# Optimization experiments

Hardware: AMD Instinct MI355X
Metric: run time of the kernel (lower is better)

Reference implementation:

```python
import jax, jax.numpy as jnp
import numpy as np

B, S, E, H = 2, 2048, 1024, 16
HD = E // H
DFF = 4 * E
LN_EPS = 1e-5


def _layernorm(x, g, b):
    mu = jnp.mean(x, axis=-1, keepdims=True)
    var = jnp.mean(jnp.square(x - mu), axis=-1, keepdims=True)
    return (x - mu) * jax.lax.rsqrt(var + LN_EPS) * g + b


def setup_inputs() -> dict:
    key = jax.random.key(0)
    ks = jax.random.split(key, 6)
    inp = {
        "x": jax.random.normal(ks[0], (B, S, E), jnp.float32),
        "ln1_g": jnp.ones((E,), jnp.float32),
        "ln1_b": jnp.zeros((E,), jnp.float32),
        "ln2_g": jnp.ones((E,), jnp.float32),
        "ln2_b": jnp.zeros((E,), jnp.float32),
        # OptimizedPoincareBallLinear init: randn * 0.1, zero bias
        "w_qkv": jax.random.normal(ks[1], (3 * E, E), jnp.float32) * 0.1,
        "b_qkv": jnp.zeros((3 * E,), jnp.float32),
        "w_ao": jax.random.normal(ks[2], (E, E), jnp.float32) * 0.1,
        "b_ao": jnp.zeros((E,), jnp.float32),
        "w_fc": jax.random.normal(ks[3], (DFF, E), jnp.float32) * 0.1,
        "b_fc": jnp.zeros((DFF,), jnp.float32),
        "w_po": jax.random.normal(ks[4], (E, DFF), jnp.float32) * 0.1,
        "b_po": jnp.zeros((E,), jnp.float32),
    }
    return inp


def reference(x, ln1_g, ln1_b, ln2_g, ln2_b, w_qkv, b_qkv, w_ao, b_ao,
              w_fc, b_fc, w_po, b_po):
    # --- attention branch ---
    h = _layernorm(x, ln1_g, ln1_b)
    qkv = h @ w_qkv.T + b_qkv                       # [B,S,3E]
    qkv = qkv.reshape(B, S, H, 3 * HD).transpose(0, 2, 1, 3)  # [B,H,S,3hd]
    q, k, v = jnp.split(qkv, 3, axis=-1)            # each [B,H,S,hd]
    scores = jnp.einsum('bhqd,bhkd->bhqk', q, k) / jnp.sqrt(
        jnp.asarray(HD, jnp.float32))
    causal = jnp.tril(jnp.ones((S, S), bool))        # attn_bias[:, :, :S, :S]
    scores = jnp.where(causal, scores, jnp.finfo(scores.dtype).min)
    attn_w = jax.nn.softmax(scores, axis=-1)         # dropout p=0.1 inactive (eval)
    attn = jnp.einsum('bhqk,bhkd->bhqd', attn_w, v)  # [B,H,S,hd]
    attn = attn.transpose(0, 2, 1, 3).reshape(B, S, E)
    attn = attn @ w_ao.T + b_ao
    x = x + attn
    # --- MLP branch ---
    h2 = _layernorm(x, ln2_g, ln2_b)
    h2 = h2 @ w_fc.T + b_fc
    h2 = jax.nn.gelu(h2, approximate=True)           # GPT-2 gelu_new
    h2 = h2 @ w_po.T + b_po
    x = x + h2
    return x
```

## Files before the change

### kernel.cpp

```cpp
#include <hip/hip_runtime.h>
#include <cstddef>
#include <cstdint>

#define Bc 2
#define Sc 2048
#define Ec 1024
#define Hc 16
#define HDc 64
#define DFFc 4096
#define ROWS (Bc * Sc)

typedef _Float16 half8v __attribute__((ext_vector_type(8)));
typedef _Float16 half4v __attribute__((ext_vector_type(4)));
typedef float f32x4 __attribute__((ext_vector_type(4)));
typedef _Float16 h16;

__device__ inline void gld_lds16(const void* g, void* l) {
    __builtin_amdgcn_global_load_lds(
        (const __attribute__((address_space(1))) void*)g,
        (__attribute__((address_space(3))) void*)l, 16, 0, 0);
}

__device__ inline float gelu_new(float x) {
    float u = 1.5957691216057308f * fmaf(0.044715f * x * x, x, x);
    return x / (1.0f + __expf(-u));
}

__global__ __launch_bounds__(256) void cvt_kernel(const float* __restrict__ in,
                                                  h16* __restrict__ out, int n) {
    int i = (blockIdx.x * 256 + threadIdx.x) * 4;
    float4 v = *(const float4*)(in + i);
    half4v o;
    o.x = (h16)v.x; o.y = (h16)v.y; o.z = (h16)v.z; o.w = (h16)v.w;
    *(half4v*)(out + i) = o;
}

__device__ inline float block_sum256(float v, float* sb) {
    #pragma unroll
    for (int o = 32; o > 0; o >>= 1) v += __shfl_down(v, o, 64);
    int lane = threadIdx.x & 63, w = threadIdx.x >> 6;
    if (lane == 0) sb[w] = v;
    __syncthreads();
    float r = sb[0] + sb[1] + sb[2] + sb[3];
    __syncthreads();
    return r;
}

__global__ __launch_bounds__(256) void ln_kernel(const float* __restrict__ x,
                                                 const float* __restrict__ g,
                                                 const float* __restrict__ b,
                                                 h16* __restrict__ out) {
    __shared__ float sb[4];
    int row = blockIdx.x;
    int t = threadIdx.x;
    const float* xr = x + (size_t)row * Ec;
    float4 v = ((const float4*)xr)[t];
    float s = v.x + v.y + v.z + v.w;
    float mu = block_sum256(s, sb) * (1.0f / Ec);
    float dx = v.x - mu, dy = v.y - mu, dz = v.z - mu, dw = v.w - mu;
    float ss = dx * dx + dy * dy + dz * dz + dw * dw;
    float var = block_sum256(ss, sb) * (1.0f / Ec);
    float inv = rsqrtf(var + 1e-5f);
    float4 gv = ((const float4*)g)[t];
    float4 bv = ((const float4*)b)[t];
    half4v o;
    o.x = (h16)(dx * inv * gv.x + bv.x);
    o.y = (h16)(dy * inv * gv.y + bv.y);
    o.z = (h16)(dz * inv * gv.z + bv.z);
    o.w = (h16)(dw * inv * gv.w + bv.w);
    ((half4v*)(out + (size_t)row * Ec))[t] = o;
}

template <int EPI, typename OutT>
__global__ __launch_bounds__(256) void gemm_mfma(
    const h16* __restrict__ A, const h16* __restrict__ W,
    const float* __restrict__ bias, const float* __restrict__ R,
    OutT* __restrict__ C, int M, int N, int K)
{
    __shared__ h16 As[2][128 * 32];
    __shared__ h16 Ws[2][128 * 32];

    const int t = threadIdx.x;
    const int lane = t & 63, wv = t >> 6;
    const int wm = wv >> 1, wn = wv & 1;
    const int c15 = lane & 15, q = lane >> 4;
    const int row0 = blockIdx.y * 128, col0 = blockIdx.x * 128;
    const int arow = t >> 2, acol = (t & 3) << 3;

    f32x4 acc[4][4];
    #pragma unroll
    for (int i = 0; i < 4; ++i)
        #pragma unroll
        for (int j = 0; j < 4; ++j)
            acc[i][j] = (f32x4){0.f, 0.f, 0.f, 0.f};

    for (int k0 = 0; k0 < K; k0 += 64) {
        __syncthreads();
        #pragma unroll
        for (int kk = 0; kk < 2; ++kk)
            #pragma unroll
            for (int p = 0; p < 2; ++p) {
                int r = p * 64 + arow;
                gld_lds16(A + (size_t)(row0 + r) * K + k0 + kk * 32 + acol,
                          &As[kk][r * 32 + acol]);
                gld_lds16(W + (size_t)(col0 + r) * K + k0 + kk * 32 + acol,
                          &Ws[kk][r * 32 + acol]);
            }
        __syncthreads();

        #pragma unroll
        for (int kk = 0; kk < 2; ++kk) {
            half8v af[4], bf[4];
            #pragma unroll
            for (int i = 0; i < 4; ++i)
                af[i] = *(const half8v*)&As[kk][(wm * 64 + i * 16 + c15) * 32 + q * 8];
            #pragma unroll
            for (int j = 0; j < 4; ++j)
                bf[j] = *(const half8v*)&Ws[kk][(wn * 64 + j * 16 + c15) * 32 + q * 8];
            #pragma unroll
            for (int i = 0; i < 4; ++i)
                #pragma unroll
                for (int j = 0; j < 4; ++j)
                    acc[i][j] = __builtin_amdgcn_mfma_f32_16x16x32_f16(af[i], bf[j], acc[i][j], 0, 0, 0);
        }
    }

    #pragma unroll
    for (int i = 0; i < 4; ++i) {
        #pragma unroll
        for (int j = 0; j < 4; ++j) {
            int col = col0 + wn * 64 + j * 16 + c15;
            float bv = bias[col];
            #pragma unroll
            for (int r = 0; r < 4; ++r) {
                int row = row0 + wm * 64 + i * 16 + q * 4 + r;
                size_t off = (size_t)row * N + col;
                float v = acc[i][j][r] + bv;
                if (EPI == 1) v += R[off];
                if (EPI == 2) v = gelu_new(v);
                if (sizeof(OutT) == 2) ((h16*)C)[off] = (h16)v;
                else ((float*)C)[off] = v;
            }
        }
    }
}

template <int EPI, typename OutT>
__global__ __launch_bounds__(256) void gemm_k64(
    const h16* __restrict__ A, const h16* __restrict__ W,
    const float* __restrict__ bias, const float* __restrict__ R,
    OutT* __restrict__ C, int M, int N, int K)
{
    __shared__ h16 As[4][64 * 32];
    __shared__ h16 Ws[4][128 * 32];

    const int t = threadIdx.x;
    const int lane = t & 63, wv = t >> 6;
    const int wm = wv >> 1, wn = wv & 1;
    const int c15 = lane & 15, q = lane >> 4;
    const int row0 = blockIdx.y * 64, col0 = blockIdx.x * 128;
    const int arow = t >> 2, acol = (t & 3) << 3;

    f32x4 acc[2][4];
    #pragma unroll
    for (int i = 0; i < 2; ++i)
        #pragma unroll
        for (int j = 0; j < 4; ++j)
            acc[i][j] = (f32x4){0.f, 0.f, 0.f, 0.f};

    for (int k0 = 0; k0 < K; k0 += 128) {
        __syncthreads();
        #pragma unroll
        for (int kk = 0; kk < 4; ++kk) {
            gld_lds16(A + (size_t)(row0 + arow) * K + k0 + kk * 32 + acol,
                      &As[kk][arow * 32 + acol]);
            #pragma unroll
            for (int p = 0; p < 2; ++p) {
                int r = p * 64 + arow;
                gld_lds16(W + (size_t)(col0 + r) * K + k0 + kk * 32 + acol,
                          &Ws[kk][r * 32 + acol]);
            }
        }
        __syncthreads();

        #pragma unroll
        for (int kk = 0; kk < 4; ++kk) {
            half8v af[2], bf[4];
            #pragma unroll
            for (int i = 0; i < 2; ++i)
                af[i] = *(const half8v*)&As[kk][(wm * 32 + i * 16 + c15) * 32 + q * 8];
            #pragma unroll
            for (int j = 0; j < 4; ++j)
                bf[j] = *(const half8v*)&Ws[kk][(wn * 64 + j * 16 + c15) * 32 + q * 8];
            #pragma unroll
            for (int i = 0; i < 2; ++i)
                #pragma unroll
                for (int j = 0; j < 4; ++j)
                    acc[i][j] = __builtin_amdgcn_mfma_f32_16x16x32_f16(af[i], bf[j], acc[i][j], 0, 0, 0);
        }
    }

    #pragma unroll
    for (int i = 0; i < 2; ++i) {
        #pragma unroll
        for (int j = 0; j < 4; ++j) {
            int col = col0 + wn * 64 + j * 16 + c15;
            float bv = bias[col];
            #pragma unroll
            for (int r = 0; r < 4; ++r) {
                int row = row0 + wm * 32 + i * 16 + q * 4 + r;
                size_t off = (size_t)row * N + col;
                float v = acc[i][j][r] + bv;
                if (EPI == 1) v += R[off];
                if (EPI == 2) v = gelu_new(v);
                if (sizeof(OutT) == 2) ((h16*)C)[off] = (h16)v;
                else ((float*)C)[off] = v;
            }
        }
    }
}

__global__ __launch_bounds__(256, 4) void attn_mfma(const h16* __restrict__ qkv,
                                                    h16* __restrict__ attn) {
    __shared__ h16 Ks[2][2][64 * 32];
    __shared__ h16 Vt[2][64 * 32];
    __shared__ h16 Ps[4][16 * 72];

    const int t = threadIdx.x;
    const int lane = t & 63, wv = t >> 6;
    const int c15 = lane & 15, q = lane >> 4;
    const int bh = blockIdx.x, b = bh >> 4, h = bh & 15;
    const int ja = 31 - blockIdx.y;
    const int qbase = ja * 64 + wv * 16;
    const int SE = 3 * Ec;
    const size_t hbase = (size_t)b * Sc * SE + (size_t)h * (3 * HDc);

    half8v qf[2];
    #pragma unroll
    for (int kk = 0; kk < 2; ++kk) {
        qf[kk] = *(const half8v*)(qkv + hbase + (size_t)(qbase + c15) * SE + kk * 32 + q * 8);
        qf[kk] *= (h16)0.125f;
    }

    f32x4 O[4];
    #pragma unroll
    for (int n = 0; n < 4; ++n) O[n] = (f32x4){0.f, 0.f, 0.f, 0.f};
    float mi = -3e38f, li = 0.f;

    const int krow = t >> 2, kcol = (t & 3) << 3;
    const int vkey = t & 31, vd0 = (t >> 5) << 3;
    half8v vreg[2];

    auto stageK = [&](int kt, int bf) {
        #pragma unroll
        for (int p = 0; p < 2; ++p)
            gld_lds16(qkv + hbase + (size_t)(kt * 64 + krow) * SE + HDc + p * 32 + kcol,
                      &Ks[bf][p][krow * 32 + kcol]);
    };
    auto loadV = [&](int kt) {
        #pragma unroll
        for (int p = 0; p < 2; ++p)
            vreg[p] = *(const half8v*)(qkv + hbase +
                        (size_t)(kt * 64 + p * 32 + vkey) * SE + 2 * HDc + vd0);
    };
    auto scatV = [&]() {
        #pragma unroll
        for (int p = 0; p < 2; ++p)
            #pragma unroll
            for (int u = 0; u < 8; ++u)
                Vt[p][(vd0 + u) * 32 + vkey] = vreg[p][u];
    };

    stageK(0, 0);
    loadV(0);
    scatV();
    __syncthreads();

    for (int kt = 0; kt <= ja; ++kt) {
        const int bf = kt & 1;
        if (kt < ja) { stageK(kt + 1, bf ^ 1); loadV(kt + 1); }

        f32x4 st[4];
        #pragma unroll
        for (int j = 0; j < 4; ++j) {
            half8v kf0 = *(const half8v*)&Ks[bf][0][(j * 16 + c15) * 32 + q * 8];
            half8v kf1 = *(const half8v*)&Ks[bf][1][(j * 16 + c15) * 32 + q * 8];
            f32x4 z = (f32x4){0.f, 0.f, 0.f, 0.f};
            z = __builtin_amdgcn_mfma_f32_16x16x32_f16(kf0, qf[0], z, 0, 0, 0);
            st[j] = __builtin_amdgcn_mfma_f32_16x16x32_f16(kf1, qf[1], z, 0, 0, 0);
        }

        if (kt == ja) {
            const int rowloc = wv * 16 + c15;
            #pragma unroll
            for (int j = 0; j < 4; ++j)
                #pragma unroll
                for (int r = 0; r < 4; ++r)
                    if (j * 16 + q * 4 + r > rowloc) st[j][r] = -3e38f;
        }

        float mx = mi;
        #pragma unroll
        for (int j = 0; j < 4; ++j)
            #pragma unroll
            for (int r = 0; r < 4; ++r) mx = fmaxf(mx, st[j][r]);
        mx = fmaxf(mx, __shfl_xor(mx, 16, 64));
        mx = fmaxf(mx, __shfl_xor(mx, 32, 64));
        float al = __expf(mi - mx);
        mi = mx;
        float ps = 0.f;
        #pragma unroll
        for (int j = 0; j < 4; ++j) {
            half4v pk;
            #pragma unroll
            for (int r = 0; r < 4; ++r) {
                float p = __expf(st[j][r] - mx);
                ps += p;
                pk[r] = (h16)p;
            }
            *(half4v*)&Ps[wv][c15 * 72 + j * 16 + q * 4] = pk;
        }
        ps += __shfl_xor(ps, 16, 64);
        ps += __shfl_xor(ps, 32, 64);
        li = li * al + ps;

        half8v pb0 = *(const half8v*)&Ps[wv][c15 * 72 + q * 8];
        half8v pb1 = *(const half8v*)&Ps[wv][c15 * 72 + 32 + q * 8];
        #pragma unroll
        for (int n = 0; n < 4; ++n) {
            #pragma unroll
            for (int r = 0; r < 4; ++r) O[n][r] *= al;
            half8v va0 = *(const half8v*)&Vt[0][(n * 16 + c15) * 32 + q * 8];
            half8v va1 = *(const half8v*)&Vt[1][(n * 16 + c15) * 32 + q * 8];
            O[n] = __builtin_amdgcn_mfma_f32_16x16x32_f16(va0, pb0, O[n], 0, 0, 0);
            O[n] = __builtin_amdgcn_mfma_f32_16x16x32_f16(va1, pb1, O[n], 0, 0, 0);
        }

        if (kt < ja) {
            __syncthreads();
            scatV();
            __syncthreads();
        }
    }

    float rl = 1.0f / li;
    #pragma unroll
    for (int n = 0; n < 4; ++n) {
        half4v o4;
        #pragma unroll
        for (int r = 0; r < 4; ++r) o4[r] = (h16)(O[n][r] * rl);
        *(half4v*)(attn + ((size_t)(b * Sc + qbase + c15)) * Ec + h * HDc + n * 16 + q * 4) = o4;
    }
}

extern "C" void kernel_launch(void* const* d_in, const int* in_sizes, int n_in,
                              void* d_out, int out_size, void* d_ws, size_t ws_size,
                              hipStream_t stream) {
    const float* x     = (const float*)d_in[0];
    const float* ln1_g = (const float*)d_in[1];
    const float* ln1_b = (const float*)d_in[2];
    const float* ln2_g = (const float*)d_in[3];
    const float* ln2_b = (const float*)d_in[4];
    const float* w_qkv = (const float*)d_in[5];
    const float* b_qkv = (const float*)d_in[6];
    const float* w_ao  = (const float*)d_in[7];
    const float* b_ao  = (const float*)d_in[8];
    const float* w_fc  = (const float*)d_in[9];
    const float* b_fc  = (const float*)d_in[10];
    const float* w_po  = (const float*)d_in[11];
    const float* b_po  = (const float*)d_in[12];
    float* out = (float*)d_out;

    char* w = (char*)d_ws;
    h16* wqkv = (h16*)(w);
    h16* wao  = (h16*)(w + 6291456);
    h16* wfc  = (h16*)(w + 8388608);
    h16* wpo  = (h16*)(w + 16777216);
    h16* hb   = (h16*)(w + 25165824);
    h16* qkv  = (h16*)(w + 33554432);
    h16* attn = (h16*)(w + 58720256);
    float* x1 = (float*)(w + 67108864);
    h16* ff   = qkv;

    dim3 blk(256);

    cvt_kernel<<<dim3(3 * Ec * Ec / 1024), blk, 0, stream>>>(w_qkv, wqkv, 3 * Ec * Ec);
    cvt_kernel<<<dim3(Ec * Ec / 1024), blk, 0, stream>>>(w_ao, wao, Ec * Ec);
    cvt_kernel<<<dim3(DFFc * Ec / 1024), blk, 0, stream>>>(w_fc, wfc, DFFc * Ec);
    cvt_kernel<<<dim3(Ec * DFFc / 1024), blk, 0, stream>>>(w_po, wpo, Ec * DFFc);

    ln_kernel<<<dim3(ROWS), blk, 0, stream>>>(x, ln1_g, ln1_b, hb);
    gemm_mfma<0, h16><<<dim3(3 * Ec / 128, ROWS / 128), blk, 0, stream>>>(
        hb, wqkv, b_qkv, nullptr, qkv, ROWS, 3 * Ec, Ec);
    attn_mfma<<<dim3(Bc * Hc, 32), blk, 0, stream>>>(qkv, attn);
    gemm_k64<1, float><<<dim3(Ec / 128, ROWS / 64), blk, 0, stream>>>(
        attn, wao, b_ao, x, x1, ROWS, Ec, Ec);
    ln_kernel<<<dim3(ROWS), blk, 0, stream>>>(x1, ln2_g, ln2_b, hb);
    gemm_mfma<2, h16><<<dim3(DFFc / 128, ROWS / 128), blk, 0, stream>>>(
        hb, wfc, b_fc, nullptr, ff, ROWS, DFFc, Ec);
    gemm_k64<1, float><<<dim3(Ec / 128, ROWS / 64), blk, 0, stream>>>(
        ff, wpo, b_po, x1, out, ROWS, Ec, DFFc);
}
```

Measured before the change: 352.3 us.

## Merge weight conversions, hoist GEMM address math, remap k64 block order

Replaces the four weight-conversion launches with a single kernel that dispatches on block index, cutting launch overhead. Both GEMMs now precompute global and LDS pointers once and advance them per K step instead of recomputing full addresses each iteration. The k64 GEMM uses a 1D grid with a swizzled block-to-tile mapping that groups 8 row tiles per column group, aiming for better L2 reuse. The GELU polynomial is refactored to save a multiply. The main risks are the hardcoded offsets and the swizzle, which assumes 64 row tiles and 8 column tiles.

```diff
diff --git a/kernel.cpp b/kernel.cpp
--- a/kernel.cpp
+++ b/kernel.cpp
@@ -22,17 +22,31 @@
 }
 
 __device__ inline float gelu_new(float x) {
-    float u = 1.5957691216057308f * fmaf(0.044715f * x * x, x, x);
+    float x2 = x * x;
+    float u = x * fmaf(0.07135481627362f, x2, 1.5957691216057308f);
     return x / (1.0f + __expf(-u));
 }
 
-__global__ __launch_bounds__(256) void cvt_kernel(const float* __restrict__ in,
-                                                  h16* __restrict__ out, int n) {
-    int i = (blockIdx.x * 256 + threadIdx.x) * 4;
-    float4 v = *(const float4*)(in + i);
+__global__ __launch_bounds__(256) void cvt4_kernel(
+    const float* __restrict__ a,
+    const float* __restrict__ b,
+    const float* __restrict__ c,
+    const float* __restrict__ d,
+    h16* __restrict__ out)
+{
+    int bid = blockIdx.x;
+    const float* src;
+    size_t obase;
+    int base;
+    if (bid < 3072)      { src = a; obase = 0;       base = bid; }
+    else if (bid < 4096) { src = b; obase = 3145728; base = bid - 3072; }
+    else if (bid < 8192) { src = c; obase = 4194304; base = bid - 4096; }
+    else                 { src = d; obase = 8388608; base = bid - 8192; }
+    int i = base * 1024 + threadIdx.x * 4;
+    float4 v = *(const float4*)(src + i);
     half4v o;
     o.x = (h16)v.x; o.y = (h16)v.y; o.z = (h16)v.z; o.w = (h16)v.w;
-    *(half4v*)(out + i) = o;
+    *(half4v*)(out + obase + i) = o;
 }
 
 __device__ inline float block_sum256(float v, float* sb) {
@@ -87,6 +101,19 @@
     const int row0 = blockIdx.y * 128, col0 = blockIdx.x * 128;
     const int arow = t >> 2, acol = (t & 3) << 3;
 
+    const h16* ap0 = A + (size_t)(row0 + arow) * K + acol;
+    const h16* ap1 = ap0 + (size_t)64 * K;
+    const h16* wp0 = W + (size_t)(col0 + arow) * K + acol;
+    const h16* wp1 = wp0 + (size_t)64 * K;
+    h16* lA0[2]; h16* lA1[2]; h16* lW0[2]; h16* lW1[2];
+    #pragma unroll
+    for (int kk = 0; kk < 2; ++kk) {
+        lA0[kk] = &As[kk][arow * 32 + acol];
+        lA1[kk] = &As[kk][(64 + arow) * 32 + acol];
+        lW0[kk] = &Ws[kk][arow * 32 + acol];
+        lW1[kk] = &Ws[kk][(64 + arow) * 32 + acol];
+    }
+
     f32x4 acc[4][4];
     #pragma unroll
     for (int i = 0; i < 4; ++i)
@@ -97,15 +124,12 @@
     for (int k0 = 0; k0 < K; k0 += 64) {
         __syncthreads();
         #pragma unroll
-        for (int kk = 0; kk < 2; ++kk)
-            #pragma unroll
-            for (int p = 0; p < 2; ++p) {
-                int r = p * 64 + arow;
-                gld_lds16(A + (size_t)(row0 + r) * K + k0 + kk * 32 + acol,
-                          &As[kk][r * 32 + acol]);
-                gld_lds16(W + (size_t)(col0 + r) * K + k0 + kk * 32 + acol,
-                          &Ws[kk][r * 32 + acol]);
-            }
+        for (int kk = 0; kk < 2; ++kk) {
+            gld_lds16(ap0 + kk * 32, lA0[kk]);
+            gld_lds16(ap1 + kk * 32, lA1[kk]);
+            gld_lds16(wp0 + kk * 32, lW0[kk]);
+            gld_lds16(wp1 + kk * 32, lW1[kk]);
+        }
         __syncthreads();
 
         #pragma unroll
@@ -123,6 +147,7 @@
                 for (int j = 0; j < 4; ++j)
                     acc[i][j] = __builtin_amdgcn_mfma_f32_16x16x32_f16(af[i], bf[j], acc[i][j], 0, 0, 0);
         }
+        ap0 += 64; ap1 += 64; wp0 += 64; wp1 += 64;
     }
 
     #pragma unroll
@@ -158,8 +183,24 @@
     const int lane = t & 63, wv = t >> 6;
     const int wm = wv >> 1, wn = wv & 1;
     const int c15 = lane & 15, q = lane >> 4;
-    const int row0 = blockIdx.y * 64, col0 = blockIdx.x * 128;
+    const int id = blockIdx.x;
+    const int cx = id & 7;
+    const int kq = id >> 3;
+    const int bx = kq & 7;
+    const int by = ((kq >> 3) << 3) | cx;
+    const int row0 = by * 64, col0 = bx * 128;
     const int arow = t >> 2, acol = (t & 3) << 3;
+
+    const h16* ap  = A + (size_t)(row0 + arow) * K + acol;
+    const h16* wp0 = W + (size_t)(col0 + arow) * K + acol;
+    const h16* wp1 = wp0 + (size_t)64 * K;
+    h16* lA[4]; h16* lW0[4]; h16* lW1[4];
+    #pragma unroll
+    for (int kk = 0; kk < 4; ++kk) {
+        lA[kk]  = &As[kk][arow * 32 + acol];
+        lW0[kk] = &Ws[kk][arow * 32 + acol];
+        lW1[kk] = &Ws[kk][(64 + arow) * 32 + acol];
+    }
 
     f32x4 acc[2][4];
     #pragma unroll
@@ -172,14 +213,9 @@
         __syncthreads();
         #pragma unroll
         for (int kk = 0; kk < 4; ++kk) {
-            gld_lds16(A + (size_t)(row0 + arow) * K + k0 + kk * 32 + acol,
-                      &As[kk][arow * 32 + acol]);
-            #pragma unroll
-            for (int p = 0; p < 2; ++p) {
-                int r = p * 64 + arow;
-                gld_lds16(W + (size_t)(col0 + r) * K + k0 + kk * 32 + acol,
-                          &Ws[kk][r * 32 + acol]);
-            }
+            gld_lds16(ap  + kk * 32, lA[kk]);
+            gld_lds16(wp0 + kk * 32, lW0[kk]);
+            gld_lds16(wp1 + kk * 32, lW1[kk]);
         }
         __syncthreads();
 
@@ -198,6 +234,7 @@
                 for (int j = 0; j < 4; ++j)
                     acc[i][j] = __builtin_amdgcn_mfma_f32_16x16x32_f16(af[i], bf[j], acc[i][j], 0, 0, 0);
         }
+        ap += 128; wp0 += 128; wp1 += 128;
     }
 
     #pragma unroll
@@ -384,20 +421,17 @@
 
     dim3 blk(256);
 
-    cvt_kernel<<<dim3(3 * Ec * Ec / 1024), blk, 0, stream>>>(w_qkv, wqkv, 3 * Ec * Ec);
-    cvt_kernel<<<dim3(Ec * Ec / 1024), blk, 0, stream>>>(w_ao, wao, Ec * Ec);
-    cvt_kernel<<<dim3(DFFc * Ec / 1024), blk, 0, stream>>>(w_fc, wfc, DFFc * Ec);
-    cvt_kernel<<<dim3(Ec * DFFc / 1024), blk, 0, stream>>>(w_po, wpo, Ec * DFFc);
+    cvt4_kernel<<<dim3(12288), blk, 0, stream>>>(w_qkv, w_ao, w_fc, w_po, wqkv);
 
     ln_kernel<<<dim3(ROWS), blk, 0, stream>>>(x, ln1_g, ln1_b, hb);
     gemm_mfma<0, h16><<<dim3(3 * Ec / 128, ROWS / 128), blk, 0, stream>>>(
         hb, wqkv, b_qkv, nullptr, qkv, ROWS, 3 * Ec, Ec);
     attn_mfma<<<dim3(Bc * Hc, 32), blk, 0, stream>>>(qkv, attn);
-    gemm_k64<1, float><<<dim3(Ec / 128, ROWS / 64), blk, 0, stream>>>(
+    gemm_k64<1, float><<<dim3(512), blk, 0, stream>>>(
         attn, wao, b_ao, x, x1, ROWS, Ec, Ec);
     ln_kernel<<<dim3(ROWS), blk, 0, stream>>>(x1, ln2_g, ln2_b, hb);
     gemm_mfma<2, h16><<<dim3(DFFc / 128, ROWS / 128), blk, 0, stream>>>(
         hb, wfc, b_fc, nullptr, ff, ROWS, DFFc, Ec);
-    gemm_k64<1, float><<<dim3(Ec / 128, ROWS / 64), blk, 0, stream>>>(
+    gemm_k64<1, float><<<dim3(512), blk, 0, stream>>>(
         ff, wpo, b_po, x1, out, ROWS, Ec, DFFc);
 }
```

Measured after the change: 345.3 us. 1.02x faster.
